# Optimization experiments

Measured on AMD Instinct MI355X. Metric: run time of the kernel, lower is better.

The kernel has to match this reference:

```python
import jax, jax.numpy as jnp
import numpy as np

NUM_HEADS = 4


def setup_inputs() -> dict:
    key = jax.random.key(0)
    ks = jax.random.split(key, 12)
    N, E_edges, ND, ED, D, G = 50000, 800000, 128, 64, 256, 128
    h = jax.random.normal(ks[0], (N, ND), dtype=jnp.float32)
    edge_index = jax.random.randint(ks[1], (2, E_edges), 0, N)
    edge_attr = jax.random.normal(ks[2], (E_edges, ED), dtype=jnp.float32)
    batch = jnp.sort(jax.random.randint(ks[3], (N,), 0, G))
    node_w = jax.random.normal(ks[4], (D, ND), dtype=jnp.float32) / np.sqrt(ND)
    node_b = jnp.zeros((D,), dtype=jnp.float32)
    edge_w = jax.random.normal(ks[5], (D, ED), dtype=jnp.float32) / np.sqrt(ED)
    edge_b = jnp.zeros((D,), dtype=jnp.float32)
    query = jax.random.normal(ks[6], (1, D), dtype=jnp.float32)
    in_w = jax.random.normal(ks[7], (3 * D, D), dtype=jnp.float32) / np.sqrt(D)
    in_b = jnp.zeros((3 * D,), dtype=jnp.float32)
    out_w = jax.random.normal(ks[8], (D, D), dtype=jnp.float32) / np.sqrt(D)
    out_b = jnp.zeros((D,), dtype=jnp.float32)
    return {"h": h, "edge_index": edge_index, "edge_attr": edge_attr, "batch": batch,
            "num_graphs": G, "node_w": node_w, "node_b": node_b,
            "edge_w": edge_w, "edge_b": edge_b, "query": query,
            "in_w": in_w, "in_b": in_b, "out_w": out_w, "out_b": out_b}


def reference(h, edge_index, edge_attr, batch, num_graphs,
              node_w, node_b, edge_w, edge_b, query, in_w, in_b, out_w, out_b):
    N = h.shape[0]
    D = query.shape[-1]
    dh = D // NUM_HEADS
    G = num_graphs
    # node projection
    h_proj = h @ node_w.T + node_b  # [N, D]
    # scatter-mean edge features to source nodes
    row = edge_index[0]
    e_proj = edge_attr @ edge_w.T + edge_b  # [E, D]
    e_sum = jax.ops.segment_sum(e_proj, row, num_segments=N)
    cnt = jax.ops.segment_sum(jnp.ones((row.shape[0],), jnp.float32), row, num_segments=N)
    h_proj = h_proj + e_sum / jnp.maximum(cnt, 1.0)[:, None]
    # per-graph single-query multi-head attention (torch MultiheadAttention math)
    wq, wk, wv = in_w[:D], in_w[D:2 * D], in_w[2 * D:]
    bq, bk, bv = in_b[:D], in_b[D:2 * D], in_b[2 * D:]
    q = (query @ wq.T + bq).reshape(NUM_HEADS, dh)            # [H, dh]
    k = (h_proj @ wk.T + bk).reshape(N, NUM_HEADS, dh)        # [N, H, dh]
    v = (h_proj @ wv.T + bv).reshape(N, NUM_HEADS, dh)        # [N, H, dh]
    scores = jnp.einsum('hd,nhd->nh', q, k) / jnp.sqrt(jnp.float32(dh))  # [N, H]
    smax = jax.ops.segment_max(scores, batch, num_segments=G)  # [G, H]
    w = jnp.exp(scores - smax[batch])                          # [N, H]
    denom = jax.ops.segment_sum(w, batch, num_segments=G)      # [G, H]
    p = w / jnp.maximum(denom[batch], 1e-30)                   # [N, H]
    pooled = jax.ops.segment_sum(p[:, :, None] * v, batch, num_segments=G)  # [G, H, dh]
    out = pooled.reshape(G, 1, D) @ out_w.T + out_b            # [G, 1, D]
    return out
```

## Files before the change

kernel.cpp:

```cpp
#include <hip/hip_runtime.h>
#include <hip/hip_bf16.h>
#include <math.h>

#define NDIM 128
#define EDIM 64
#define DDIM 256
#define NSPLIT 4
#define CAP 96
#define AGS 72

typedef __attribute__((ext_vector_type(8))) short short8;

__device__ inline ushort f2bf(float x) {
    uint32_t u = __float_as_uint(x);
    uint32_t r = (u + 0x7fff + ((u >> 16) & 1)) >> 16;
    return (ushort)r;
}
__device__ inline float bf2f(ushort h) { return __uint_as_float(((uint32_t)h) << 16); }

__global__ __launch_bounds__(256) void k_setup(
    int* __restrict__ zero_p, int n_zero, int ZBLK,
    const float* __restrict__ node_w, const float* __restrict__ edge_w,
    const float* __restrict__ node_b, const float* __restrict__ edge_b,
    const float* __restrict__ query, const float* __restrict__ in_w,
    const float* __restrict__ in_b, float* __restrict__ prep)
{
    const int tid = threadIdx.x;
    int b = blockIdx.x;
    if (b < ZBLK) {
        int i = b * 256 + tid;
        if (i < n_zero) zero_p[i] = 0;
        return;
    }
    __shared__ float q_s[DDIM];
    __shared__ float qv[DDIM];
    __shared__ float qk_s[4 * DDIM];
    __shared__ float sb_s[4];
    q_s[tid] = query[tid];
    __syncthreads();
    float acc = in_b[tid];
    const float* wq = in_w + (size_t)tid * DDIM;
    for (int i = 0; i < DDIM; ++i) acc += q_s[i] * wq[i];
    qv[tid] = acc;
    __syncthreads();
    for (int h = 0; h < 4; ++h) {
        float a = 0.f;
        for (int d = 0; d < 64; ++d)
            a += qv[h * 64 + d] * in_w[(size_t)(DDIM + h * 64 + d) * DDIM + tid];
        qk_s[h * DDIM + tid] = a;
    }
    if (tid < 4) {
        float a = 0.f;
        for (int d = 0; d < 64; ++d) a += qv[tid * 64 + d] * in_b[DDIM + tid * 64 + d];
        sb_s[tid] = a;
    }
    __syncthreads();
    for (int idx = tid; idx < 4 * NDIM; idx += 256) {
        int hh = idx >> 7, k = idx & 127;
        float a = 0.f;
        for (int j = 0; j < DDIM; ++j) a += qk_s[hh * DDIM + j] * node_w[(size_t)j * NDIM + k];
        prep[idx] = a;
    }
    {
        int hh = tid >> 6, k = tid & 63;
        float a = 0.f;
        for (int j = 0; j < DDIM; ++j) a += qk_s[hh * DDIM + j] * edge_w[(size_t)j * EDIM + k];
        prep[4 * NDIM + tid] = a;
    }
    if (tid < 4) {
        float a = 0.f, e = 0.f;
        for (int j = 0; j < DDIM; ++j) {
            a += node_b[j] * qk_s[tid * DDIM + j];
            e += edge_b[j] * qk_s[tid * DDIM + j];
        }
        prep[4 * NDIM + 256 + tid] = a + sb_s[tid];
        prep[4 * NDIM + 260 + tid] = e;
    }
}

__global__ __launch_bounds__(256) void k_scatbin(
    const int* __restrict__ erow, const float* __restrict__ edge_attr,
    int* __restrict__ fill, ushort* __restrict__ ebin, int E)
{
    int gid = blockIdx.x * 256 + threadIdx.x;
    int e = gid >> 3;
    int seg8 = gid & 7;
    if (e >= E) return;
    int r = erow[e];
    int pos = 0;
    if (seg8 == 0) pos = atomicAdd(&fill[r], 1);
    pos = __shfl(pos, 0, 8);
    if (pos >= CAP) return;
    const float* ea = edge_attr + (size_t)e * EDIM + seg8 * 8;
    float4 va = *reinterpret_cast<const float4*>(ea);
    float4 vb = *reinterpret_cast<const float4*>(ea + 4);
    short8 o;
    o[0] = (short)f2bf(va.x); o[1] = (short)f2bf(va.y);
    o[2] = (short)f2bf(va.z); o[3] = (short)f2bf(va.w);
    o[4] = (short)f2bf(vb.x); o[5] = (short)f2bf(vb.y);
    o[6] = (short)f2bf(vb.z); o[7] = (short)f2bf(vb.w);
    *reinterpret_cast<short8*>(
        ebin + ((size_t)r * CAP + pos) * EDIM + seg8 * 8) = o;
}

__global__ __launch_bounds__(256) void k_poolscore(
    const float* __restrict__ h, const ushort* __restrict__ ebin,
    const int* __restrict__ fill, const float* __restrict__ prep,
    const int* __restrict__ batch,
    float* __restrict__ pm, float* __restrict__ pdn, float* __restrict__ pe,
    float* __restrict__ pv, float* __restrict__ pu, int N)
{
    __shared__ ushort agg_s[256 * AGS];
    __shared__ float sc_s[256 * 4];
    __shared__ float cn_s[256];
    __shared__ float qkn_s[4 * NDIM];
    __shared__ float qke_s[4 * EDIM];
    __shared__ float cst[8];
    __shared__ float red_a[16];
    __shared__ float red_b[16];
    __shared__ float vred[2][4][NDIM];
    __shared__ float ured[4][4][EDIM];

    const int b = blockIdx.x;
    const int g = b >> 2;
    const int part = b & 3;
    const int tid = threadIdx.x;
    const int lane = tid & 63;
    const int wave = tid >> 6;
    const int dv = tid & 127;
    const int g2 = tid >> 7;
    const int du = tid & 63;
    const int g4 = tid >> 6;
    const int seg8 = tid & 7;

    for (int i = tid; i < 4 * NDIM; i += 256) qkn_s[i] = prep[i];
    qke_s[tid] = prep[4 * NDIM + tid];
    if (tid < 8) cst[tid] = prep[4 * NDIM + 256 + tid];

    int lo = 0, hi = N;
    while (lo < hi) { int mid = (lo + hi) >> 1; if (batch[mid] < g) lo = mid + 1; else hi = mid; }
    const int s = lo;
    hi = N;
    while (lo < hi) { int mid = (lo + hi) >> 1; if (batch[mid] < g + 1) lo = mid + 1; else hi = mid; }
    const int e = lo;
    const int len = e - s;
    const int cs = s + (len * part) / NSPLIT;
    const int ce = s + (len * (part + 1)) / NSPLIT;

    float m[4], dn[4], spe[4], v[4], uh[4];
#pragma unroll
    for (int hh = 0; hh < 4; ++hh) {
        m[hh] = -INFINITY; dn[hh] = 0.f; spe[hh] = 0.f; v[hh] = 0.f; uh[hh] = 0.f;
    }

    const int hsel = tid & 3;

    for (int c = cs; c < ce; c += 256) {
        int cn = min(256, ce - c);
        __syncthreads();
        if (tid < cn) cn_s[tid] = (float)fill[c + tid];
        __syncthreads();

        for (int pass = 0; pass < 8; ++pass) {
            int node_l = pass * 32 + (tid >> 3);
            if (node_l < cn) {
                int n = c + node_l;
                float cntf = cn_s[node_l];
                int ci = min((int)cntf, CAP);
                float inv = 1.f / fmaxf(cntf, 1.f);
                float fl = (cntf > 0.5f) ? 1.f : 0.f;

                float hd[4] = {0.f, 0.f, 0.f, 0.f};
                const float4* hp = reinterpret_cast<const float4*>(
                    h + (size_t)n * NDIM + seg8 * 16);
#pragma unroll
                for (int q = 0; q < 4; ++q) {
                    float4 hv = hp[q];
                    int bq = seg8 * 16 + q * 4;
#pragma unroll
                    for (int hh = 0; hh < 4; ++hh) {
                        const float* qp = &qkn_s[hh * NDIM + bq];
                        hd[hh] += hv.x * qp[0] + hv.y * qp[1] + hv.z * qp[2] + hv.w * qp[3];
                    }
                }

                float a[8];
#pragma unroll
                for (int i = 0; i < 8; ++i) a[i] = 0.f;
                {
                    const ushort* eb = ebin + ((size_t)n * CAP) * EDIM + seg8 * 8;
                    int j = 0;
                    for (; j + 3 < ci; j += 4) {
                        short8 v0 = *reinterpret_cast<const short8*>(eb + (size_t)(j + 0) * EDIM);
                        short8 v1 = *reinterpret_cast<const short8*>(eb + (size_t)(j + 1) * EDIM);
                        short8 v2 = *reinterpret_cast<const short8*>(eb + (size_t)(j + 2) * EDIM);
                        short8 v3 = *reinterpret_cast<const short8*>(eb + (size_t)(j + 3) * EDIM);
#pragma unroll
                        for (int i = 0; i < 8; ++i)
                            a[i] += (bf2f((ushort)v0[i]) + bf2f((ushort)v1[i]))
                                  + (bf2f((ushort)v2[i]) + bf2f((ushort)v3[i]));
                    }
                    for (; j < ci; ++j) {
                        short8 v0 = *reinterpret_cast<const short8*>(eb + (size_t)j * EDIM);
#pragma unroll
                        for (int i = 0; i < 8; ++i) a[i] += bf2f((ushort)v0[i]);
                    }
                }
                {
                    short8 o;
#pragma unroll
                    for (int i = 0; i < 8; ++i) o[i] = (short)f2bf(a[i]);
                    *reinterpret_cast<short8*>(&agg_s[node_l * AGS + seg8 * 8]) = o;
                }
                float ed[4] = {0.f, 0.f, 0.f, 0.f};
#pragma unroll
                for (int i = 0; i < 8; ++i) {
#pragma unroll
                    for (int hh = 0; hh < 4; ++hh)
                        ed[hh] += a[i] * qke_s[hh * EDIM + seg8 * 8 + i];
                }
                float t[4];
#pragma unroll
                for (int hh = 0; hh < 4; ++hh) t[hh] = hd[hh] + ed[hh] * inv;
#pragma unroll
                for (int off = 1; off < 8; off <<= 1) {
#pragma unroll
                    for (int hh = 0; hh < 4; ++hh) t[hh] += __shfl_xor(t[hh], off);
                }
                if (seg8 == 0) {
                    float4 sc;
                    sc.x = (t[0] + cst[0] + fl * cst[4]) * 0.125f;
                    sc.y = (t[1] + cst[1] + fl * cst[5]) * 0.125f;
                    sc.z = (t[2] + cst[2] + fl * cst[6]) * 0.125f;
                    sc.w = (t[3] + cst[3] + fl * cst[7]) * 0.125f;
                    *reinterpret_cast<float4*>(&sc_s[node_l * 4]) = sc;
                }
            }
        }
        __syncthreads();

        float lm = -INFINITY;
        for (int n = tid >> 2; n < cn; n += 64) lm = fmaxf(lm, sc_s[n * 4 + hsel]);
#pragma unroll
        for (int off = 4; off < 64; off <<= 1) lm = fmaxf(lm, __shfl_xor(lm, off));
        if (lane < 4) red_a[wave * 4 + lane] = lm;
        __syncthreads();

        float nm[4];
#pragma unroll
        for (int hh = 0; hh < 4; ++hh) {
            float cm = fmaxf(fmaxf(red_a[hh], red_a[4 + hh]),
                             fmaxf(red_a[8 + hh], red_a[12 + hh]));
            nm[hh] = fmaxf(m[hh], cm);
            float sc = expf(m[hh] - nm[hh]);
            dn[hh] *= sc; spe[hh] *= sc; v[hh] *= sc; uh[hh] *= sc;
            m[hh] = nm[hh];
        }
        __syncthreads();

        float mh = (hsel == 0) ? nm[0] : (hsel == 1) ? nm[1] : (hsel == 2) ? nm[2] : nm[3];
        float ld = 0.f, le = 0.f;
        for (int idx = tid; idx < cn * 4; idx += 256) {
            float wv = expf(sc_s[idx] - mh);
            sc_s[idx] = wv;
            ld += wv;
            le += wv * ((cn_s[idx >> 2] > 0.5f) ? 1.f : 0.f);
        }
#pragma unroll
        for (int off = 4; off < 64; off <<= 1) {
            ld += __shfl_xor(ld, off);
            le += __shfl_xor(le, off);
        }
        if (lane < 4) { red_a[wave * 4 + lane] = ld; red_b[wave * 4 + lane] = le; }
        __syncthreads();
#pragma unroll
        for (int hh = 0; hh < 4; ++hh) {
            dn[hh]  += red_a[hh] + red_a[4 + hh] + red_a[8 + hh] + red_a[12 + hh];
            spe[hh] += red_b[hh] + red_b[4 + hh] + red_b[8 + hh] + red_b[12 + hh];
        }

        for (int ln = g2; ln < cn; ln += 2) {
            float val = h[(size_t)(c + ln) * NDIM + dv];
            float4 w4 = *reinterpret_cast<const float4*>(&sc_s[ln * 4]);
            v[0] += w4.x * val; v[1] += w4.y * val;
            v[2] += w4.z * val; v[3] += w4.w * val;
        }
        for (int ln = g4; ln < cn; ln += 4) {
            float val = bf2f(agg_s[ln * AGS + du]);
            float ci = 1.f / fmaxf(cn_s[ln], 1.f);
            float4 w4 = *reinterpret_cast<const float4*>(&sc_s[ln * 4]);
            uh[0] += w4.x * ci * val; uh[1] += w4.y * ci * val;
            uh[2] += w4.z * ci * val; uh[3] += w4.w * ci * val;
        }
    }

    __syncthreads();
#pragma unroll
    for (int hh = 0; hh < 4; ++hh) {
        vred[g2][hh][dv] = v[hh];
        ured[g4][hh][du] = uh[hh];
    }
    __syncthreads();

    if (tid < 4) { pm[b * 4 + tid] = m[tid]; pdn[b * 4 + tid] = dn[tid]; pe[b * 4 + tid] = spe[tid]; }
    for (int idx = tid; idx < 4 * NDIM; idx += 256) {
        int hh = idx >> 7, k = idx & 127;
        pv[(size_t)(b * 4 + hh) * NDIM + k] = vred[0][hh][k] + vred[1][hh][k];
    }
    {
        int hh = tid >> 6, k = tid & 63;
        pu[(size_t)(b * 4 + hh) * EDIM + k] =
            ured[0][hh][k] + ured[1][hh][k] + ured[2][hh][k] + ured[3][hh][k];
    }
}

__global__ __launch_bounds__(256) void k_out(
    const float* __restrict__ pm, const float* __restrict__ pdn, const float* __restrict__ pe,
    const float* __restrict__ pv, const float* __restrict__ pu,
    const float* __restrict__ node_w, const float* __restrict__ edge_w,
    const float* __restrict__ node_b, const float* __restrict__ edge_b,
    const float* __restrict__ in_w, const float* __restrict__ in_b,
    const float* __restrict__ out_w, const float* __restrict__ out_b,
    float* __restrict__ out)
{
    __shared__ float vm[4][NDIM];
    __shared__ float um[4][EDIM];
    __shared__ float scp_s[NSPLIT][4];
    __shared__ float dnm_s[4];
    __shared__ float spe_s[4];
    __shared__ float has_s;
    __shared__ float hb_s[4 * DDIM];
    __shared__ float po_s[DDIM];

    const int g = blockIdx.x;
    const int tid = threadIdx.x;
    const int b0 = NSPLIT * g;

    if (tid < 4) {
        float Mh = -INFINITY;
#pragma unroll
        for (int p = 0; p < NSPLIT; ++p) Mh = fmaxf(Mh, pm[(b0 + p) * 4 + tid]);
        float d = 0.f, ee = 0.f;
#pragma unroll
        for (int p = 0; p < NSPLIT; ++p) {
            float mp = pm[(b0 + p) * 4 + tid];
            float scp = (mp == -INFINITY) ? 0.f : expf(mp - Mh);
            scp_s[p][tid] = scp;
            d += pdn[(b0 + p) * 4 + tid] * scp;
            ee += pe[(b0 + p) * 4 + tid] * scp;
        }
        dnm_s[tid] = d;
        spe_s[tid] = ee;
        if (tid == 0) has_s = (Mh > -INFINITY) ? 1.f : 0.f;
    }
    __syncthreads();

    for (int idx = tid; idx < 4 * NDIM; idx += 256) {
        int hh = idx >> 7, k = idx & 127;
        float a = 0.f;
#pragma unroll
        for (int p = 0; p < NSPLIT; ++p)
            a += pv[(size_t)((b0 + p) * 4 + hh) * NDIM + k] * scp_s[p][hh];
        vm[hh][k] = a;
    }
    {
        int hh = tid >> 6, k = tid & 63;
        float a = 0.f;
#pragma unroll
        for (int p = 0; p < NSPLIT; ++p)
            a += pu[(size_t)((b0 + p) * 4 + hh) * EDIM + k] * scp_s[p][hh];
        um[hh][k] = a;
    }
    __syncthreads();

    {
        int j = tid;
        float acch[4];
        float nbj = node_b[j], ebj = edge_b[j];
#pragma unroll
        for (int hh = 0; hh < 4; ++hh) acch[hh] = dnm_s[hh] * nbj + spe_s[hh] * ebj;
        const float4* nwr = reinterpret_cast<const float4*>(node_w + (size_t)j * NDIM);
        for (int q = 0; q < NDIM / 4; ++q) {
            float4 w4 = nwr[q];
#pragma unroll
            for (int hh = 0; hh < 4; ++hh) {
                const float* vp = &vm[hh][q * 4];
                acch[hh] += w4.x * vp[0] + w4.y * vp[1] + w4.z * vp[2] + w4.w * vp[3];
            }
        }
        const float4* ewr = reinterpret_cast<const float4*>(edge_w + (size_t)j * EDIM);
        for (int q = 0; q < EDIM / 4; ++q) {
            float4 w4 = ewr[q];
#pragma unroll
            for (int hh = 0; hh < 4; ++hh) {
                const float* up = &um[hh][q * 4];
                acch[hh] += w4.x * up[0] + w4.y * up[1] + w4.z * up[2] + w4.w * up[3];
            }
        }
#pragma unroll
        for (int hh = 0; hh < 4; ++hh)
            hb_s[hh * DDIM + j] = acch[hh] / fmaxf(dnm_s[hh], 1e-30f);
    }
    __syncthreads();

    const int jh = tid >> 6;
    const float* wv_row = in_w + (size_t)(2 * DDIM + tid) * DDIM;
    const float* hbr = &hb_s[jh * DDIM];
    float p = 0.f;
    for (int i = 0; i < DDIM; i += 4) {
        float4 a = *reinterpret_cast<const float4*>(hbr + i);
        float4 bb = *reinterpret_cast<const float4*>(wv_row + i);
        p += a.x * bb.x + a.y * bb.y + a.z * bb.z + a.w * bb.w;
    }
    p = (p + in_b[2 * DDIM + tid]) * has_s;
    po_s[tid] = p;
    __syncthreads();

    const float* ow_row = out_w + (size_t)tid * DDIM;
    float o = out_b[tid];
    for (int i = 0; i < DDIM; i += 4) {
        float4 a = *reinterpret_cast<const float4*>(&po_s[i]);
        float4 bb = *reinterpret_cast<const float4*>(ow_row + i);
        o += a.x * bb.x + a.y * bb.y + a.z * bb.z + a.w * bb.w;
    }
    out[(size_t)g * DDIM + tid] = o;
}

extern "C" void kernel_launch(void* const* d_in, const int* in_sizes, int n_in,
                              void* d_out, int out_size, void* d_ws, size_t ws_size,
                              hipStream_t stream) {
    const float* h         = (const float*)d_in[0];
    const int*   edge_idx  = (const int*)d_in[1];
    const float* edge_attr = (const float*)d_in[2];
    const int*   batch     = (const int*)d_in[3];
    const float* node_w    = (const float*)d_in[5];
    const float* node_b    = (const float*)d_in[6];
    const float* edge_w    = (const float*)d_in[7];
    const float* edge_b    = (const float*)d_in[8];
    const float* query     = (const float*)d_in[9];
    const float* in_w      = (const float*)d_in[10];
    const float* in_b      = (const float*)d_in[11];
    const float* out_w     = (const float*)d_in[12];
    const float* out_b     = (const float*)d_in[13];
    float* out = (float*)d_out;

    const int N = in_sizes[0] / NDIM;
    const int E = in_sizes[2] / EDIM;
    const int G = out_size / DDIM;

    char* ws = (char*)d_ws;
    size_t off = 0;
    auto alloc = [&](size_t bytes) { void* p = ws + off; off += (bytes + 255) & ~(size_t)255; return p; };

    int*    fill    = (int*)alloc((size_t)N * 4);
    float*  prep    = (float*)alloc(776 * 4);
    float*  pm      = (float*)alloc((size_t)NSPLIT * G * 4 * 4);
    float*  pdn     = (float*)alloc((size_t)NSPLIT * G * 4 * 4);
    float*  pe      = (float*)alloc((size_t)NSPLIT * G * 4 * 4);
    float*  pv      = (float*)alloc((size_t)NSPLIT * G * 4 * NDIM * 4);
    float*  pu      = (float*)alloc((size_t)NSPLIT * G * 4 * EDIM * 4);
    ushort* ebin    = (ushort*)alloc((size_t)N * CAP * EDIM * 2);

    const int ZBLK = (N + 255) / 256;
    k_setup<<<ZBLK + 1, 256, 0, stream>>>(
        fill, N, ZBLK, node_w, edge_w, node_b, edge_b, query, in_w, in_b, prep);

    k_scatbin<<<((E * 8) + 255) / 256, 256, 0, stream>>>(
        edge_idx, edge_attr, fill, ebin, E);

    k_poolscore<<<NSPLIT * G, 256, 0, stream>>>(
        h, ebin, fill, prep, batch, pm, pdn, pe, pv, pu, N);

    k_out<<<G, 256, 0, stream>>>(
        pm, pdn, pe, pv, pu, node_w, edge_w, node_b, edge_b,
        in_w, in_b, out_w, out_b, out);
}
```

Before: 186.3 us.

## Fuse setup, scatter, pooling and output into one cooperative megakernel

Merges the four separate kernels (zero/setup, edge binning scatter, per-graph pooled scoring, final projection) into a single cooperative kernel that uses grid-wide syncs between phases. It runs 512 blocks and uses grid-stride loops for the zeroing and scatter phases. The aim is to remove the launch and drain gaps between kernels. In exchange, the scatter phase loses the much larger grid it had before, and grid syncs add their own cost. The old multi-kernel path remains as a fallback if a cooperative launch is not possible.

```diff
diff --git a/kernel.cpp b/kernel.cpp
--- a/kernel.cpp
+++ b/kernel.cpp
@@ -1,6 +1,9 @@
 #include <hip/hip_runtime.h>
 #include <hip/hip_bf16.h>
+#include <hip/hip_cooperative_groups.h>
 #include <math.h>
+
+namespace cg = cooperative_groups;
 
 #define NDIM 128
 #define EDIM 64
@@ -17,6 +20,392 @@
     return (ushort)r;
 }
 __device__ inline float bf2f(ushort h) { return __uint_as_float(((uint32_t)h) << 16); }
+
+__global__ __launch_bounds__(256, 2) void k_mega(
+    const float* __restrict__ h, const int* __restrict__ erow,
+    const float* __restrict__ edge_attr, const int* __restrict__ batch,
+    const float* __restrict__ node_w, const float* __restrict__ node_b,
+    const float* __restrict__ edge_w, const float* __restrict__ edge_b,
+    const float* __restrict__ query, const float* __restrict__ in_w,
+    const float* __restrict__ in_b, const float* __restrict__ out_w,
+    const float* __restrict__ out_b,
+    int* __restrict__ fill, float* __restrict__ prep,
+    float* __restrict__ pm, float* __restrict__ pdn, float* __restrict__ pe,
+    float* __restrict__ pv, float* __restrict__ pu,
+    ushort* __restrict__ ebin, float* __restrict__ out,
+    int N, int E, int G)
+{
+    cg::grid_group gridg = cg::this_grid();
+    const int tid = threadIdx.x;
+    const int bid = blockIdx.x;
+    const int gsize = gridDim.x * 256;
+    const int gidx = bid * 256 + tid;
+
+    __shared__ float q_s[DDIM], qv[DDIM], qk_s[4 * DDIM], sb_s[4];
+    __shared__ ushort agg_s[256 * AGS];
+    __shared__ float sc_s[256 * 4], cn_s[256];
+    __shared__ float qkn_s[4 * NDIM], qke_s[4 * EDIM], cst[8];
+    __shared__ float red_a[16], red_b[16];
+    __shared__ float vred[2][4][NDIM], ured[4][4][EDIM];
+    __shared__ float vm[4][NDIM], um[4][EDIM];
+    __shared__ float scp_s[NSPLIT][4], dnm_s[4], spe_s[4], has_s;
+    __shared__ float hb_s[4 * DDIM], po_s[DDIM];
+
+    for (int i = gidx; i < N; i += gsize) fill[i] = 0;
+    if (bid == gridDim.x - 1) {
+        q_s[tid] = query[tid];
+        __syncthreads();
+        float acc = in_b[tid];
+        const float* wq = in_w + (size_t)tid * DDIM;
+        for (int i = 0; i < DDIM; ++i) acc += q_s[i] * wq[i];
+        qv[tid] = acc;
+        __syncthreads();
+        for (int hh = 0; hh < 4; ++hh) {
+            float a = 0.f;
+            for (int d = 0; d < 64; ++d)
+                a += qv[hh * 64 + d] * in_w[(size_t)(DDIM + hh * 64 + d) * DDIM + tid];
+            qk_s[hh * DDIM + tid] = a;
+        }
+        if (tid < 4) {
+            float a = 0.f;
+            for (int d = 0; d < 64; ++d) a += qv[tid * 64 + d] * in_b[DDIM + tid * 64 + d];
+            sb_s[tid] = a;
+        }
+        __syncthreads();
+        for (int idx = tid; idx < 4 * NDIM; idx += 256) {
+            int hh = idx >> 7, k = idx & 127;
+            float a = 0.f;
+            for (int j = 0; j < DDIM; ++j) a += qk_s[hh * DDIM + j] * node_w[(size_t)j * NDIM + k];
+            prep[idx] = a;
+        }
+        {
+            int hh = tid >> 6, k = tid & 63;
+            float a = 0.f;
+            for (int j = 0; j < DDIM; ++j) a += qk_s[hh * DDIM + j] * edge_w[(size_t)j * EDIM + k];
+            prep[4 * NDIM + tid] = a;
+        }
+        if (tid < 4) {
+            float a = 0.f, e = 0.f;
+            for (int j = 0; j < DDIM; ++j) {
+                a += node_b[j] * qk_s[tid * DDIM + j];
+                e += edge_b[j] * qk_s[tid * DDIM + j];
+            }
+            prep[4 * NDIM + 256 + tid] = a + sb_s[tid];
+            prep[4 * NDIM + 260 + tid] = e;
+        }
+    }
+    gridg.sync();
+
+    {
+        const int total = E * 8;
+        for (int it = gidx; it < total; it += gsize) {
+            int e = it >> 3;
+            int seg8 = it & 7;
+            int r = erow[e];
+            int pos = 0;
+            if (seg8 == 0) pos = atomicAdd(&fill[r], 1);
+            pos = __shfl(pos, 0, 8);
+            if (pos < CAP) {
+                const float* ea = edge_attr + (size_t)e * EDIM + seg8 * 8;
+                float4 va = *reinterpret_cast<const float4*>(ea);
+                float4 vb = *reinterpret_cast<const float4*>(ea + 4);
+                short8 o;
+                o[0] = (short)f2bf(va.x); o[1] = (short)f2bf(va.y);
+                o[2] = (short)f2bf(va.z); o[3] = (short)f2bf(va.w);
+                o[4] = (short)f2bf(vb.x); o[5] = (short)f2bf(vb.y);
+                o[6] = (short)f2bf(vb.z); o[7] = (short)f2bf(vb.w);
+                *reinterpret_cast<short8*>(
+                    ebin + ((size_t)r * CAP + pos) * EDIM + seg8 * 8) = o;
+            }
+        }
+    }
+    gridg.sync();
+
+    {
+        const int gno = bid >> 2;
+        const int part = bid & 3;
+        const int lane = tid & 63;
+        const int wave = tid >> 6;
+        const int dv = tid & 127;
+        const int g2 = tid >> 7;
+        const int du = tid & 63;
+        const int g4 = tid >> 6;
+        const int seg8 = tid & 7;
+
+        for (int i = tid; i < 4 * NDIM; i += 256) qkn_s[i] = prep[i];
+        qke_s[tid] = prep[4 * NDIM + tid];
+        if (tid < 8) cst[tid] = prep[4 * NDIM + 256 + tid];
+        __syncthreads();
+
+        int lo = 0, hi = N;
+        while (lo < hi) { int mid = (lo + hi) >> 1; if (batch[mid] < gno) lo = mid + 1; else hi = mid; }
+        const int s = lo;
+        hi = N;
+        while (lo < hi) { int mid = (lo + hi) >> 1; if (batch[mid] < gno + 1) lo = mid + 1; else hi = mid; }
+        const int e = lo;
+        const int len = e - s;
+        const int cs = s + (len * part) / NSPLIT;
+        const int ce = s + (len * (part + 1)) / NSPLIT;
+
+        float m[4], dn[4], spe[4], v[4], uh[4];
+#pragma unroll
+        for (int hh = 0; hh < 4; ++hh) {
+            m[hh] = -INFINITY; dn[hh] = 0.f; spe[hh] = 0.f; v[hh] = 0.f; uh[hh] = 0.f;
+        }
+        const int hsel = tid & 3;
+
+        for (int c = cs; c < ce; c += 256) {
+            int cn = min(256, ce - c);
+            __syncthreads();
+            if (tid < cn) cn_s[tid] = (float)fill[c + tid];
+            __syncthreads();
+
+            for (int pass = 0; pass < 8; ++pass) {
+                int node_l = pass * 32 + (tid >> 3);
+                if (node_l < cn) {
+                    int n = c + node_l;
+                    float cntf = cn_s[node_l];
+                    int ci = min((int)cntf, CAP);
+                    float inv = 1.f / fmaxf(cntf, 1.f);
+                    float fl = (cntf > 0.5f) ? 1.f : 0.f;
+
+                    float hd[4] = {0.f, 0.f, 0.f, 0.f};
+                    const float4* hp = reinterpret_cast<const float4*>(
+                        h + (size_t)n * NDIM + seg8 * 16);
+#pragma unroll
+                    for (int q = 0; q < 4; ++q) {
+                        float4 hv = hp[q];
+                        int bq = seg8 * 16 + q * 4;
+#pragma unroll
+                        for (int hh = 0; hh < 4; ++hh) {
+                            const float* qp = &qkn_s[hh * NDIM + bq];
+                            hd[hh] += hv.x * qp[0] + hv.y * qp[1] + hv.z * qp[2] + hv.w * qp[3];
+                        }
+                    }
+
+                    float a[8];
+#pragma unroll
+                    for (int i = 0; i < 8; ++i) a[i] = 0.f;
+                    {
+                        const ushort* eb = ebin + ((size_t)n * CAP) * EDIM + seg8 * 8;
+                        int j = 0;
+                        for (; j + 3 < ci; j += 4) {
+                            short8 v0 = *reinterpret_cast<const short8*>(eb + (size_t)(j + 0) * EDIM);
+                            short8 v1 = *reinterpret_cast<const short8*>(eb + (size_t)(j + 1) * EDIM);
+                            short8 v2 = *reinterpret_cast<const short8*>(eb + (size_t)(j + 2) * EDIM);
+                            short8 v3 = *reinterpret_cast<const short8*>(eb + (size_t)(j + 3) * EDIM);
+#pragma unroll
+                            for (int i = 0; i < 8; ++i)
+                                a[i] += (bf2f((ushort)v0[i]) + bf2f((ushort)v1[i]))
+                                      + (bf2f((ushort)v2[i]) + bf2f((ushort)v3[i]));
+                        }
+                        for (; j < ci; ++j) {
+                            short8 v0 = *reinterpret_cast<const short8*>(eb + (size_t)j * EDIM);
+#pragma unroll
+                            for (int i = 0; i < 8; ++i) a[i] += bf2f((ushort)v0[i]);
+                        }
+                    }
+                    {
+                        short8 o;
+#pragma unroll
+                        for (int i = 0; i < 8; ++i) o[i] = (short)f2bf(a[i]);
+                        *reinterpret_cast<short8*>(&agg_s[node_l * AGS + seg8 * 8]) = o;
+                    }
+                    float ed[4] = {0.f, 0.f, 0.f, 0.f};
+#pragma unroll
+                    for (int i = 0; i < 8; ++i) {
+#pragma unroll
+                        for (int hh = 0; hh < 4; ++hh)
+                            ed[hh] += a[i] * qke_s[hh * EDIM + seg8 * 8 + i];
+                    }
+                    float t[4];
+#pragma unroll
+                    for (int hh = 0; hh < 4; ++hh) t[hh] = hd[hh] + ed[hh] * inv;
+#pragma unroll
+                    for (int off = 1; off < 8; off <<= 1) {
+#pragma unroll
+                        for (int hh = 0; hh < 4; ++hh) t[hh] += __shfl_xor(t[hh], off);
+                    }
+                    if (seg8 == 0) {
+                        float4 sc;
+                        sc.x = (t[0] + cst[0] + fl * cst[4]) * 0.125f;
+                        sc.y = (t[1] + cst[1] + fl * cst[5]) * 0.125f;
+                        sc.z = (t[2] + cst[2] + fl * cst[6]) * 0.125f;
+                        sc.w = (t[3] + cst[3] + fl * cst[7]) * 0.125f;
+                        *reinterpret_cast<float4*>(&sc_s[node_l * 4]) = sc;
+                    }
+                }
+            }
+            __syncthreads();
+
+            float lm = -INFINITY;
+            for (int n = tid >> 2; n < cn; n += 64) lm = fmaxf(lm, sc_s[n * 4 + hsel]);
+#pragma unroll
+            for (int off = 4; off < 64; off <<= 1) lm = fmaxf(lm, __shfl_xor(lm, off));
+            if (lane < 4) red_a[wave * 4 + lane] = lm;
+            __syncthreads();
+
+            float nm[4];
+#pragma unroll
+            for (int hh = 0; hh < 4; ++hh) {
+                float cm = fmaxf(fmaxf(red_a[hh], red_a[4 + hh]),
+                                 fmaxf(red_a[8 + hh], red_a[12 + hh]));
+                nm[hh] = fmaxf(m[hh], cm);
+                float sc = expf(m[hh] - nm[hh]);
+                dn[hh] *= sc; spe[hh] *= sc; v[hh] *= sc; uh[hh] *= sc;
+                m[hh] = nm[hh];
+            }
+            __syncthreads();
+
+            float mh = (hsel == 0) ? nm[0] : (hsel == 1) ? nm[1] : (hsel == 2) ? nm[2] : nm[3];
+            float ld = 0.f, le = 0.f;
+            for (int idx = tid; idx < cn * 4; idx += 256) {
+                float wv = expf(sc_s[idx] - mh);
+                sc_s[idx] = wv;
+                ld += wv;
+                le += wv * ((cn_s[idx >> 2] > 0.5f) ? 1.f : 0.f);
+            }
+#pragma unroll
+            for (int off = 4; off < 64; off <<= 1) {
+                ld += __shfl_xor(ld, off);
+                le += __shfl_xor(le, off);
+            }
+            if (lane < 4) { red_a[wave * 4 + lane] = ld; red_b[wave * 4 + lane] = le; }
+            __syncthreads();
+#pragma unroll
+            for (int hh = 0; hh < 4; ++hh) {
+                dn[hh]  += red_a[hh] + red_a[4 + hh] + red_a[8 + hh] + red_a[12 + hh];
+                spe[hh] += red_b[hh] + red_b[4 + hh] + red_b[8 + hh] + red_b[12 + hh];
+            }
+
+            for (int ln = g2; ln < cn; ln += 2) {
+                float val = h[(size_t)(c + ln) * NDIM + dv];
+                float4 w4 = *reinterpret_cast<const float4*>(&sc_s[ln * 4]);
+                v[0] += w4.x * val; v[1] += w4.y * val;
+                v[2] += w4.z * val; v[3] += w4.w * val;
+            }
+            for (int ln = g4; ln < cn; ln += 4) {
+                float val = bf2f(agg_s[ln * AGS + du]);
+                float ci = 1.f / fmaxf(cn_s[ln], 1.f);
+                float4 w4 = *reinterpret_cast<const float4*>(&sc_s[ln * 4]);
+                uh[0] += w4.x * ci * val; uh[1] += w4.y * ci * val;
+                uh[2] += w4.z * ci * val; uh[3] += w4.w * ci * val;
+            }
+        }
+
+        __syncthreads();
+#pragma unroll
+        for (int hh = 0; hh < 4; ++hh) {
+            vred[g2][hh][dv] = v[hh];
+            ured[g4][hh][du] = uh[hh];
+        }
+        __syncthreads();
+
+        if (tid < 4) { pm[bid * 4 + tid] = m[tid]; pdn[bid * 4 + tid] = dn[tid]; pe[bid * 4 + tid] = spe[tid]; }
+        for (int idx = tid; idx < 4 * NDIM; idx += 256) {
+            int hh = idx >> 7, k = idx & 127;
+            pv[(size_t)(bid * 4 + hh) * NDIM + k] = vred[0][hh][k] + vred[1][hh][k];
+        }
+        {
+            int hh = tid >> 6, k = tid & 63;
+            pu[(size_t)(bid * 4 + hh) * EDIM + k] =
+                ured[0][hh][k] + ured[1][hh][k] + ured[2][hh][k] + ured[3][hh][k];
+        }
+    }
+    gridg.sync();
+
+    if (bid < G) {
+        const int b0 = NSPLIT * bid;
+        if (tid < 4) {
+            float Mh = -INFINITY;
+#pragma unroll
+            for (int p = 0; p < NSPLIT; ++p) Mh = fmaxf(Mh, pm[(b0 + p) * 4 + tid]);
+            float d = 0.f, ee = 0.f;
+#pragma unroll
+            for (int p = 0; p < NSPLIT; ++p) {
+                float mp = pm[(b0 + p) * 4 + tid];
+                float scp = (mp == -INFINITY) ? 0.f : expf(mp - Mh);
+                scp_s[p][tid] = scp;
+                d += pdn[(b0 + p) * 4 + tid] * scp;
+                ee += pe[(b0 + p) * 4 + tid] * scp;
+            }
+            dnm_s[tid] = d;
+            spe_s[tid] = ee;
+            if (tid == 0) has_s = (Mh > -INFINITY) ? 1.f : 0.f;
+        }
+        __syncthreads();
+
+        for (int idx = tid; idx < 4 * NDIM; idx += 256) {
+            int hh = idx >> 7, k = idx & 127;
+            float a = 0.f;
+#pragma unroll
+            for (int p = 0; p < NSPLIT; ++p)
+                a += pv[(size_t)((b0 + p) * 4 + hh) * NDIM + k] * scp_s[p][hh];
+            vm[hh][k] = a;
+        }
+        {
+            int hh = tid >> 6, k = tid & 63;
+            float a = 0.f;
+#pragma unroll
+            for (int p = 0; p < NSPLIT; ++p)
+                a += pu[(size_t)((b0 + p) * 4 + hh) * EDIM + k] * scp_s[p][hh];
+            um[hh][k] = a;
+        }
+        __syncthreads();
+
+        {
+            int j = tid;
+            float acch[4];
+            float nbj = node_b[j], ebj = edge_b[j];
+#pragma unroll
+            for (int hh = 0; hh < 4; ++hh) acch[hh] = dnm_s[hh] * nbj + spe_s[hh] * ebj;
+            const float4* nwr = reinterpret_cast<const float4*>(node_w + (size_t)j * NDIM);
+            for (int q = 0; q < NDIM / 4; ++q) {
+                float4 w4 = nwr[q];
+#pragma unroll
+                for (int hh = 0; hh < 4; ++hh) {
+                    const float* vp = &vm[hh][q * 4];
+                    acch[hh] += w4.x * vp[0] + w4.y * vp[1] + w4.z * vp[2] + w4.w * vp[3];
+                }
+            }
+            const float4* ewr = reinterpret_cast<const float4*>(edge_w + (size_t)j * EDIM);
+            for (int q = 0; q < EDIM / 4; ++q) {
+                float4 w4 = ewr[q];
+#pragma unroll
+                for (int hh = 0; hh < 4; ++hh) {
+                    const float* up = &um[hh][q * 4];
+                    acch[hh] += w4.x * up[0] + w4.y * up[1] + w4.z * up[2] + w4.w * up[3];
+                }
+            }
+#pragma unroll
+            for (int hh = 0; hh < 4; ++hh)
+                hb_s[hh * DDIM + j] = acch[hh] / fmaxf(dnm_s[hh], 1e-30f);
+        }
+        __syncthreads();
+
+        const int jh = tid >> 6;
+        const float* wv_row = in_w + (size_t)(2 * DDIM + tid) * DDIM;
+        const float* hbr = &hb_s[jh * DDIM];
+        float p = 0.f;
+        for (int i = 0; i < DDIM; i += 4) {
+            float4 a = *reinterpret_cast<const float4*>(hbr + i);
+            float4 bb = *reinterpret_cast<const float4*>(wv_row + i);
+            p += a.x * bb.x + a.y * bb.y + a.z * bb.z + a.w * bb.w;
+        }
+        p = (p + in_b[2 * DDIM + tid]) * has_s;
+        po_s[tid] = p;
+        __syncthreads();
+
+        const float* ow_row = out_w + (size_t)tid * DDIM;
+        float o = out_b[tid];
+        for (int i = 0; i < DDIM; i += 4) {
+            float4 a = *reinterpret_cast<const float4*>(&po_s[i]);
+            float4 bb = *reinterpret_cast<const float4*>(ow_row + i);
+            o += a.x * bb.x + a.y * bb.y + a.z * bb.z + a.w * bb.w;
+        }
+        out[(size_t)bid * DDIM + tid] = o;
+    }
+}
 
 __global__ __launch_bounds__(256) void k_setup(
     int* __restrict__ zero_p, int n_zero, int ZBLK,
@@ -152,7 +541,6 @@
     for (int hh = 0; hh < 4; ++hh) {
         m[hh] = -INFINITY; dn[hh] = 0.f; spe[hh] = 0.f; v[hh] = 0.f; uh[hh] = 0.f;
     }
-
     const int hsel = tid & 3;
 
     for (int c = cs; c < ce; c += 256) {
@@ -444,9 +832,9 @@
     const float* out_b     = (const float*)d_in[13];
     float* out = (float*)d_out;
 
-    const int N = in_sizes[0] / NDIM;
-    const int E = in_sizes[2] / EDIM;
-    const int G = out_size / DDIM;
+    int N = in_sizes[0] / NDIM;
+    int E = in_sizes[2] / EDIM;
+    int G = out_size / DDIM;
 
     char* ws = (char*)d_ws;
     size_t off = 0;
@@ -461,16 +849,38 @@
     float*  pu      = (float*)alloc((size_t)NSPLIT * G * 4 * EDIM * 4);
     ushort* ebin    = (ushort*)alloc((size_t)N * CAP * EDIM * 2);
 
+    int nblk = 0;
+    hipError_t qerr = hipOccupancyMaxActiveBlocksPerMultiprocessor(&nblk, k_mega, 256, 0);
+    hipDeviceProp_t props;
+    int dev = 0;
+    hipGetDevice(&dev);
+    hipGetDeviceProperties(&props, dev);
+    const int grid_blocks = NSPLIT * G;
+    bool coop_ok = (qerr == hipSuccess) &&
+                   ((long long)nblk * props.multiProcessorCount >= grid_blocks) &&
+                   props.cooperativeLaunch;
+
+    if (coop_ok) {
+        void* args[] = {
+            (void*)&h, (void*)&edge_idx, (void*)&edge_attr, (void*)&batch,
+            (void*)&node_w, (void*)&node_b, (void*)&edge_w, (void*)&edge_b,
+            (void*)&query, (void*)&in_w, (void*)&in_b, (void*)&out_w, (void*)&out_b,
+            (void*)&fill, (void*)&prep, (void*)&pm, (void*)&pdn, (void*)&pe,
+            (void*)&pv, (void*)&pu, (void*)&ebin, (void*)&out,
+            (void*)&N, (void*)&E, (void*)&G
+        };
+        hipError_t lerr = hipLaunchCooperativeKernel(
+            k_mega, dim3(grid_blocks), dim3(256), args, 0, stream);
+        if (lerr == hipSuccess) return;
+    }
+
     const int ZBLK = (N + 255) / 256;
     k_setup<<<ZBLK + 1, 256, 0, stream>>>(
         fill, N, ZBLK, node_w, edge_w, node_b, edge_b, query, in_w, in_b, prep);
-
     k_scatbin<<<((E * 8) + 255) / 256, 256, 0, stream>>>(
         edge_idx, edge_attr, fill, ebin, E);
-
     k_poolscore<<<NSPLIT * G, 256, 0, stream>>>(
         h, ebin, fill, prep, batch, pm, pdn, pe, pv, pu, N);
-
     k_out<<<G, 256, 0, stream>>>(
         pm, pdn, pe, pv, pu, node_w, edge_w, node_b, edge_b,
         in_w, in_b, out_w, out_b, out);
```

Result: no change. 185.2 us (-0.6%).
